# Performance work log

Measured on AMD Instinct MI355X. Metric: run time of the kernel, lower is better.

The kernel has to match this reference:

```python
import jax, jax.numpy as jnp
import numpy as np

B, C, N, H = 4, 512, 2048, 8
D = C // H  # per-head depth = 64
EPS = 1e-5


def conv1x1(x, W, b):
    # x: [B, Cin, N], W: [Cout, Cin], b: [Cout]
    return jnp.einsum('oc,bcn->bon', W, x) + b[None, :, None]


def instance_norm(x):
    # normalize over length dim per (batch, channel), no affine
    mu = jnp.mean(x, axis=-1, keepdims=True)
    var = jnp.var(x, axis=-1, keepdims=True)
    return (x - mu) * jax.lax.rsqrt(var + EPS)


def _pipeline(src, tgt, Wq, bq, Wk, bk, Wv, bv, Wm, bm):
    # query from src, key/value from tgt; reshape C -> (D outer, H inner)
    q = conv1x1(src, Wq, bq).reshape(B, D, H, N)
    k = conv1x1(tgt, Wk, bk).reshape(B, D, H, N)
    v = conv1x1(tgt, Wv, bv).reshape(B, D, H, N)
    scores = jnp.einsum('bdhn,bdhm->bhnm', q, k) / jnp.sqrt(jnp.float32(D))
    probs = jax.nn.softmax(scores, axis=-1)
    out = jnp.einsum('bhnm,bdhm->bdhn', probs, v).reshape(B, C, N)
    return conv1x1(out, Wm, bm)


def _mlp(x, W1, b1, W2, b2):
    h = conv1x1(x, W1, b1)
    h = jax.nn.relu(instance_norm(h))
    return conv1x1(h, W2, b2)


def setup_inputs() -> dict:
    key = jax.random.key(0)
    ks = jax.random.split(key, 8)
    s = 0.02
    return {
        'source_features': jax.random.normal(ks[0], (B, C, N), jnp.float32),
        'target_features': jax.random.normal(ks[1], (B, C, N), jnp.float32),
        'Wq': jax.random.normal(ks[2], (C, C), jnp.float32) * s,
        'bq': jnp.zeros((C,), jnp.float32),
        'Wk': jax.random.normal(ks[3], (C, C), jnp.float32) * s,
        'bk': jnp.zeros((C,), jnp.float32),
        'Wv': jax.random.normal(ks[4], (C, C), jnp.float32) * s,
        'bv': jnp.zeros((C,), jnp.float32),
        'Wm': jax.random.normal(ks[5], (C, C), jnp.float32) * s,
        'bm': jnp.zeros((C,), jnp.float32),
        'W1': jax.random.normal(ks[6], (2 * C, 2 * C), jnp.float32) * s,
        'b1': jnp.zeros((2 * C,), jnp.float32),
        'W2': jax.random.normal(ks[7], (C, 2 * C), jnp.float32) * s,
        'b2': jnp.zeros((C,), jnp.float32),
    }


def reference(source_features, target_features, Wq, bq, Wk, bk, Wv, bv, Wm, bm, W1, b1, W2, b2):
    src, tgt = source_features, target_features
    # source update uses ORIGINAL target features
    src_att = _pipeline(src, tgt, Wq, bq, Wk, bk, Wv, bv, Wm, bm)
    src = src + _mlp(jnp.concatenate([src, src_att], axis=1), W1, b1, W2, b2)
    # target update uses the UPDATED source features (in-place semantics of original)
    tgt_att = _pipeline(tgt, src, Wq, bq, Wk, bk, Wv, bv, Wm, bm)
    tgt = tgt + _mlp(jnp.concatenate([tgt, tgt_att], axis=1), W1, b1, W2, b2)
    return src, tgt
```

## Files before the change

kernel.cpp:

```cpp
#include <hip/hip_runtime.h>

#define NN 2048
#define CC 512
#define BB 4
#define HH 8
#define DD 64
#define SCALE 0.18033688011112043f

typedef unsigned short u16;
typedef __attribute__((ext_vector_type(8))) short bf16x8;
typedef __attribute__((ext_vector_type(4))) float f32x4;

extern "C" __device__ float __ocml_native_exp2_f32(float);

__device__ inline u16 f2b(float x) {
    unsigned u = __builtin_bit_cast(unsigned, x);
    u += 0x7fffu + ((u >> 16) & 1u);
    return (u16)(u >> 16);
}
__device__ inline float b2f(u16 h) {
    unsigned u = ((unsigned)h) << 16;
    return __builtin_bit_cast(float, u);
}

#define GLD16(g, l) __builtin_amdgcn_global_load_lds( \
    (const __attribute__((address_space(1))) unsigned int*)(g), \
    (__attribute__((address_space(3))) unsigned int*)(l), 16, 0, 0)

template<int JT>
__device__ __forceinline__ void gemm_core_t(
    const u16* __restrict__ Xa, const u16* __restrict__ Xb, int Ca, int K,
    const u16* __restrict__ Wt, size_t rowBase,
    u16* As, u16* Bs, f32x4 (&acc)[4][JT])
{
    constexpr int OT = JT * 32;
    const int tid = threadIdx.x;
    const int lane = tid & 63, w = tid >> 6;
    const int quad = lane >> 4, l16 = lane & 15;
    const int wrow = w & 1, wcol = w >> 1;
    const int arow = lane >> 3, aseg = lane & 7;
    const int asw = aseg ^ arow;
    const int lk = l16 & 7;

    for (int k0 = 0; k0 < K; k0 += 64) {
        const u16* Xs; int Crow, cc;
        if (k0 < Ca) { Xs = Xa; Crow = Ca; cc = k0; }
        else         { Xs = Xb; Crow = K - Ca; cc = k0 - Ca; }
#pragma unroll
        for (int i = 0; i < 4; ++i) {
            int rl = w * 32 + i * 8 + arow;
            int la = __builtin_amdgcn_readfirstlane((w * 32 + i * 8) * 64);
            GLD16(Xs + (rowBase + rl) * (size_t)Crow + cc + asw * 8, (char*)As + (size_t)la * 2);
        }
#pragma unroll
        for (int i = 0; i < OT / 32; ++i) {
            int rl = w * (OT / 4) + i * 8 + arow;
            int la = __builtin_amdgcn_readfirstlane((w * (OT / 4) + i * 8) * 64);
            GLD16(Wt + (size_t)rl * K + k0 + asw * 8, (char*)Bs + (size_t)la * 2);
        }
        __syncthreads();
#pragma unroll
        for (int kk = 0; kk < 2; ++kk) {
            const int g = ((kk * 4 + quad) ^ lk) * 8;
            bf16x8 av[4], bv[JT];
#pragma unroll
            for (int i = 0; i < 4; ++i)
                av[i] = *(const bf16x8*)&As[(wrow * 64 + i * 16 + l16) * 64 + g];
#pragma unroll
            for (int jj = 0; jj < JT; ++jj)
                bv[jj] = *(const bf16x8*)&Bs[(wcol * JT * 16 + jj * 16 + l16) * 64 + g];
#pragma unroll
            for (int i = 0; i < 4; ++i)
#pragma unroll
                for (int jj = 0; jj < JT; ++jj)
                    acc[i][jj] = __builtin_amdgcn_mfma_f32_16x16x32_bf16(av[i], bv[jj], acc[i][jj], 0, 0, 0);
        }
        __syncthreads();
    }
}

template<int JT>
__device__ __forceinline__ void gemm_epilogue_t(
    f32x4 (&acc)[4][JT], const float* __restrict__ bias, int mode,
    int b, int n0, int o0, int Cout,
    const float* __restrict__ res, float* __restrict__ outF, u16* __restrict__ outB)
{
    const int tid = threadIdx.x;
    const int lane = tid & 63, w = tid >> 6;
    const int quad = lane >> 4, l16 = lane & 15;
    const int wrow = w & 1, wcol = w >> 1;
    const size_t bN = (size_t)b * NN;
    const int nb0 = n0 + wrow * 64, ob0 = o0 + wcol * JT * 16;

    if (mode == 0) {
#pragma unroll
        for (int j = 0; j < JT; ++j) {
            int o = ob0 + j * 16 + l16;
            float bs = bias[o];
#pragma unroll
            for (int i = 0; i < 4; ++i)
#pragma unroll
                for (int r = 0; r < 4; ++r) {
                    int n = nb0 + i * 16 + quad * 4 + r;
                    outB[(bN + n) * Cout + o] = f2b(acc[i][j][r] + bs);
                }
        }
    } else if (mode == 1) {
#pragma unroll
        for (int j = 0; j < JT; ++j) {
            int o = ob0 + j * 16 + l16;
            float bs = bias[o];
            int h = o >> 6, d = o & 63;
#pragma unroll
            for (int i = 0; i < 4; ++i) {
                int n = nb0 + i * 16 + quad * 4;
                ushort4 pk;
                pk.x = f2b(acc[i][j][0] + bs); pk.y = f2b(acc[i][j][1] + bs);
                pk.z = f2b(acc[i][j][2] + bs); pk.w = f2b(acc[i][j][3] + bs);
                *(ushort4*)&outB[(((size_t)b * HH + h) * DD + d) * NN + n] = pk;
            }
        }
    } else {
#pragma unroll
        for (int j = 0; j < JT; ++j) {
            int o = ob0 + j * 16 + l16;
            float bs = bias[o];
#pragma unroll
            for (int i = 0; i < 4; ++i) {
                int n = nb0 + i * 16 + quad * 4;
                size_t ad = ((size_t)b * Cout + o) * NN + n;
                float4 rv = *(const float4*)&res[ad];
                float4 yv;
                yv.x = acc[i][j][0] + bs + rv.x;
                yv.y = acc[i][j][1] + bs + rv.y;
                yv.z = acc[i][j][2] + bs + rv.z;
                yv.w = acc[i][j][3] + bs + rv.w;
                *(float4*)&outF[ad] = yv;
                if (mode == 2) {
                    outB[(bN + n + 0) * Cout + o] = f2b(yv.x);
                    outB[(bN + n + 1) * Cout + o] = f2b(yv.y);
                    outB[(bN + n + 2) * Cout + o] = f2b(yv.z);
                    outB[(bN + n + 3) * Cout + o] = f2b(yv.w);
                }
            }
        }
    }
}

template<int JT>
__global__ __launch_bounds__(256, (JT == 2 ? 4 : 3)) void gemm_bf16_t(
    const u16* __restrict__ Wb, const float* __restrict__ bias,
    const u16* __restrict__ Xa, const u16* __restrict__ Xb,
    int Ca, int K, int Cout,
    const float* __restrict__ res, float* __restrict__ outF,
    u16* __restrict__ outB, int mode)
{
    __shared__ u16 As[128 * 64];
    __shared__ u16 Bs[JT * 32 * 64];
    const int b = blockIdx.z, n0 = blockIdx.x * 128, o0 = blockIdx.y * (JT * 32);
    f32x4 acc[4][JT] = {};
    gemm_core_t<JT>(Xa, Xb, Ca, K, Wb + (size_t)o0 * K, (size_t)b * NN + n0, As, Bs, acc);
    gemm_epilogue_t<JT>(acc, bias, mode, b, n0, o0, Cout, res, outF, outB);
}

__global__ __launch_bounds__(256, 3) void gemm_qkv(
    const u16* __restrict__ WQ, const float* __restrict__ bQ,
    const u16* __restrict__ XQ, u16* __restrict__ outQ,
    const u16* __restrict__ WK, const float* __restrict__ bK, u16* __restrict__ outK,
    const u16* __restrict__ WV, const float* __restrict__ bV, u16* __restrict__ outV,
    const u16* __restrict__ XKV)
{
    __shared__ u16 As[128 * 64];
    __shared__ u16 Bs[128 * 64];
    const int yb = blockIdx.y;
    const u16* W; const float* bias; const u16* X; u16* outB; int mode, o0;
    if (yb < 4)      { o0 = yb * 128;       W = WQ; bias = bQ; X = XQ;  outB = outQ; mode = 0; }
    else if (yb < 8) { o0 = (yb - 4) * 128; W = WK; bias = bK; X = XKV; outB = outK; mode = 0; }
    else             { o0 = (yb - 8) * 128; W = WV; bias = bV; X = XKV; outB = outV; mode = 1; }
    const int b = blockIdx.z, n0 = blockIdx.x * 128;
    f32x4 acc[4][4] = {};
    gemm_core_t<4>(X, nullptr, 512, 512, W + (size_t)o0 * 512, (size_t)b * NN + n0, As, Bs, acc);
    gemm_epilogue_t<4>(acc, bias, mode, b, n0, o0, 512, nullptr, nullptr, outB);
}

__global__ __launch_bounds__(512, 4) void attn(
    const u16* __restrict__ Qg, const u16* __restrict__ Kg,
    const u16* __restrict__ Vg, u16* __restrict__ Og)
{
    __shared__ __align__(16) u16 pool[6 * 4096];
    u16* const Ksb[2] = { pool, pool + 4096 };
    u16* const Vtb[2] = { pool + 2 * 4096, pool + 3 * 4096 };
    u16* const Ps = pool + 4 * 4096;
    const int tid = threadIdx.x;
    const int lane = tid & 63, w = tid >> 6;
    const int qg = w & 3, hv = w >> 2;
    const int quad = lane >> 4, l16 = lane & 15;
    const int id = blockIdx.x;
    const int xcd = id & 7, jj = id >> 3;
    const int bh = xcd * 4 + (jj >> 4), nb = jj & 15;
    const int b = bh >> 3, h = bh & 7;
    const int n0 = nb * 128, wn0 = qg * 32;
    const int sr0 = w * 8;
    const size_t qkBase = ((size_t)b * NN) * CC + h * DD;
    const size_t vBase  = (((size_t)b * HH + h) * DD) * NN;
    const int r8 = lane >> 3, seg = lane & 7;
    const int segp = seg ^ r8;
    const int lk = l16 & 7;

    const u16* kp = Kg + qkBase + (size_t)(sr0 + r8) * CC + segp * 8;
    const u16* vp = Vg + vBase + (size_t)(sr0 + r8) * NN + segp * 8;

    bf16x8 qf[2][2];
#pragma unroll
    for (int qs = 0; qs < 2; ++qs) {
        int n = n0 + wn0 + qs * 16 + l16;
#pragma unroll
        for (int ks = 0; ks < 2; ++ks)
            qf[qs][ks] = *(const bf16x8*)&Qg[qkBase + (size_t)n * CC + ks * 32 + quad * 8];
    }

    const short oneb = 0x3F80;
    const bf16x8 ones = {oneb, oneb, oneb, oneb, oneb, oneb, oneb, oneb};
    f32x4 oa[2][4] = {};
    f32x4 lacc[2] = {};

    GLD16(kp, Ksb[0] + sr0 * 64);
    GLD16(vp, Vtb[0] + sr0 * 64);
    kp += 64 * CC; vp += 64;

#define ATTN_PREF(BUF) do { \
        GLD16(kp, Ksb[BUF] + sr0 * 64); \
        GLD16(vp, Vtb[BUF] + sr0 * 64); \
        kp += 64 * CC; vp += 64; \
    } while (0)

#define ATTN_BODY(CUR) do { \
        const u16* ksb = Ksb[CUR]; \
        const u16* vtb = Vtb[CUR]; \
        f32x4 st[2][2] = {}; \
        _Pragma("unroll") \
        for (int ks = 0; ks < 2; ++ks) { \
            bf16x8 ak[2]; \
            _Pragma("unroll") \
            for (int rtl = 0; rtl < 2; ++rtl) \
                ak[rtl] = *(const bf16x8*)&ksb[(hv * 32 + rtl * 16 + l16) * 64 + ((ks * 4 + quad) ^ lk) * 8]; \
            __builtin_amdgcn_s_setprio(1); \
            _Pragma("unroll") \
            for (int rtl = 0; rtl < 2; ++rtl) \
                _Pragma("unroll") \
                for (int qs = 0; qs < 2; ++qs) \
                    st[qs][rtl] = __builtin_amdgcn_mfma_f32_16x16x32_bf16(ak[rtl], qf[qs][ks], st[qs][rtl], 0, 0, 0); \
            __builtin_amdgcn_s_setprio(0); \
        } \
        _Pragma("unroll") \
        for (int qs = 0; qs < 2; ++qs) { \
            int nrow = wn0 + qs * 16 + l16; \
            _Pragma("unroll") \
            for (int rtl = 0; rtl < 2; ++rtl) { \
                unsigned u0 = __builtin_bit_cast(unsigned, __ocml_native_exp2_f32(st[qs][rtl][0])); \
                unsigned u1 = __builtin_bit_cast(unsigned, __ocml_native_exp2_f32(st[qs][rtl][1])); \
                unsigned u2 = __builtin_bit_cast(unsigned, __ocml_native_exp2_f32(st[qs][rtl][2])); \
                unsigned u3 = __builtin_bit_cast(unsigned, __ocml_native_exp2_f32(st[qs][rtl][3])); \
                uint2 t; \
                t.x = __builtin_amdgcn_perm(u1, u0, 0x07060302u); \
                t.y = __builtin_amdgcn_perm(u3, u2, 0x07060302u); \
                int g = (((hv * 2 + rtl) * 2 + (quad >> 1))) ^ lk; \
                *(uint2*)&Ps[nrow * 64 + g * 8 + (quad & 1) * 4] = t; \
            } \
        } \
        { \
            bf16x8 pa[2]; \
            _Pragma("unroll") \
            for (int qs = 0; qs < 2; ++qs) \
                pa[qs] = *(const bf16x8*)&Ps[(wn0 + qs * 16 + l16) * 64 + ((hv * 4 + quad) ^ lk) * 8]; \
            bf16x8 vb[4]; \
            _Pragma("unroll") \
            for (int ct = 0; ct < 4; ++ct) \
                vb[ct] = *(const bf16x8*)&vtb[(ct * 16 + l16) * 64 + ((hv * 4 + quad) ^ lk) * 8]; \
            __builtin_amdgcn_s_setprio(1); \
            _Pragma("unroll") \
            for (int ct = 0; ct < 4; ++ct) \
                _Pragma("unroll") \
                for (int qs = 0; qs < 2; ++qs) \
                    oa[qs][ct] = __builtin_amdgcn_mfma_f32_16x16x32_bf16(pa[qs], vb[ct], oa[qs][ct], 0, 0, 0); \
            _Pragma("unroll") \
            for (int qs = 0; qs < 2; ++qs) \
                lacc[qs] = __builtin_amdgcn_mfma_f32_16x16x32_bf16(pa[qs], ones, lacc[qs], 0, 0, 0); \
            __builtin_amdgcn_s_setprio(0); \
        } \
    } while (0)

    for (int it = 0; it < NN / 64; it += 2) {
        __syncthreads();
        ATTN_PREF(1);
        ATTN_BODY(0);
        __syncthreads();
        if (it < NN / 64 - 2)
            ATTN_PREF(0);
        ATTN_BODY(1);
    }
#undef ATTN_PREF
#undef ATTN_BODY

    __syncthreads();
    float* M = (float*)pool;
    const int mbase = (qg * 64 + lane) * 40;
    if (hv == 1) {
#pragma unroll
        for (int qs = 0; qs < 2; ++qs)
#pragma unroll
            for (int ct = 0; ct < 4; ++ct)
                *(f32x4*)&M[mbase + (qs * 4 + ct) * 4] = oa[qs][ct];
        *(f32x4*)&M[mbase + 32] = lacc[0];
        *(f32x4*)&M[mbase + 36] = lacc[1];
    }
    __syncthreads();
    if (hv == 0) {
#pragma unroll
        for (int qs = 0; qs < 2; ++qs)
#pragma unroll
            for (int ct = 0; ct < 4; ++ct)
                oa[qs][ct] += *(const f32x4*)&M[mbase + (qs * 4 + ct) * 4];
        lacc[0] += *(const f32x4*)&M[mbase + 32];
        lacc[1] += *(const f32x4*)&M[mbase + 36];
#pragma unroll
        for (int qs = 0; qs < 2; ++qs)
#pragma unroll
            for (int r = 0; r < 4; ++r) {
                float li = 1.f / lacc[qs][r];
                int n = n0 + wn0 + qs * 16 + quad * 4 + r;
#pragma unroll
                for (int ct = 0; ct < 4; ++ct)
                    Og[qkBase + (size_t)n * CC + ct * 16 + l16] = f2b(oa[qs][ct][r] * li);
            }
    }
}

__global__ __launch_bounds__(256) void transpose_cvt(
    const float* __restrict__ X, u16* __restrict__ Y)
{
    __shared__ float T[64][65];
    const int tid = threadIdx.x;
    const int n0 = blockIdx.x * 64, c0 = blockIdx.y * 64, b = blockIdx.z;
    const int rr = tid >> 4, cc4 = tid & 15;
#pragma unroll
    for (int p = 0; p < 4; ++p) {
        int cl = p * 16 + rr;
        float4 v = *(const float4*)&X[((size_t)b * CC + c0 + cl) * NN + n0 + cc4 * 4];
        T[cl][cc4 * 4 + 0] = v.x; T[cl][cc4 * 4 + 1] = v.y;
        T[cl][cc4 * 4 + 2] = v.z; T[cl][cc4 * 4 + 3] = v.w;
    }
    __syncthreads();
#pragma unroll
    for (int p = 0; p < 4; ++p) {
        int nl = p * 16 + rr;
        ushort4 pk;
        pk.x = f2b(T[cc4 * 4 + 0][nl]);
        pk.y = f2b(T[cc4 * 4 + 1][nl]);
        pk.z = f2b(T[cc4 * 4 + 2][nl]);
        pk.w = f2b(T[cc4 * 4 + 3][nl]);
        *(ushort4*)&Y[((size_t)b * NN + n0 + nl) * CC + c0 + cc4 * 4] = pk;
    }
}

__global__ __launch_bounds__(256) void prep_weights(
    const float* __restrict__ Wq, const float* __restrict__ Wk,
    const float* __restrict__ Wv, const float* __restrict__ Wm,
    const float* __restrict__ W1, const float* __restrict__ W2,
    u16* oQ, u16* oK, u16* oV, u16* oM, u16* o1, u16* o2)
{
    const float* W; u16* o; int rows, cols, perm; float sc = 1.f;
    switch (blockIdx.z) {
        case 0: W = Wq; o = oQ; rows = 512;  cols = 512;  perm = 1; sc = SCALE; break;
        case 1: W = Wk; o = oK; rows = 512;  cols = 512;  perm = 1; break;
        case 2: W = Wv; o = oV; rows = 512;  cols = 512;  perm = 1; break;
        case 3: W = Wm; o = oM; rows = 512;  cols = 512;  perm = 2; break;
        case 4: W = W1; o = o1; rows = 1024; cols = 1024; perm = 0; break;
        default: W = W2; o = o2; rows = 512; cols = 1024; perm = 0; break;
    }
    int c = blockIdx.x * 256 + threadIdx.x;
    int r = blockIdx.y;
    if (r >= rows || c >= cols) return;
    int sr = r, scol = c;
    if (perm == 1) sr = (r & 63) * 8 + (r >> 6);
    else if (perm == 2) scol = (c & 63) * 8 + (c >> 6);
    o[(size_t)r * cols + c] = f2b(W[(size_t)sr * cols + scol] * sc);
}

__global__ void prep_bias(const float* __restrict__ bq, const float* __restrict__ bk,
                          const float* __restrict__ bv,
                          float* oq, float* ok, float* ov)
{
    int i = blockIdx.x * 256 + threadIdx.x;
    int y = blockIdx.y;
    const float* s = (y == 0) ? bq : (y == 1) ? bk : bv;
    float* o = (y == 0) ? oq : (y == 1) ? ok : ov;
    float v = s[(i & 63) * 8 + (i >> 6)];
    if (y == 0) v *= SCALE;
    o[i] = v;
}

__global__ __launch_bounds__(256) void inorm_p1(
    const u16* __restrict__ X, float* __restrict__ Ssum, float* __restrict__ Ssq)
{
    __shared__ float rs[4][64], rq[4][64];
    const int tid = threadIdx.x;
    const int cl = tid & 63, g = tid >> 6;
    const int c = blockIdx.x * 64 + cl;
    const int b = blockIdx.y, nz = blockIdx.z;
    float s = 0.f, q = 0.f;
    size_t base = ((size_t)b * NN + nz * 256 + g * 64) * 1024 + c;
#pragma unroll 4
    for (int i = 0; i < 64; ++i) {
        float x = b2f(X[base + (size_t)i * 1024]);
        s += x; q += x * x;
    }
    rs[g][cl] = s; rq[g][cl] = q;
    __syncthreads();
    if (g == 0) {
        s = rs[0][cl] + rs[1][cl] + rs[2][cl] + rs[3][cl];
        q = rq[0][cl] + rq[1][cl] + rq[2][cl] + rq[3][cl];
        atomicAdd(&Ssum[b * 1024 + c], s);
        atomicAdd(&Ssq[b * 1024 + c], q);
    }
}

__global__ __launch_bounds__(256) void inorm_p2(
    u16* __restrict__ X, const float* __restrict__ Ssum, const float* __restrict__ Ssq)
{
    const int tid = threadIdx.x;
    const int cl = tid & 63, g = tid >> 6;
    const int c = blockIdx.x * 64 + cl;
    const int b = blockIdx.y, nz = blockIdx.z;
    float mean = Ssum[b * 1024 + c] * (1.f / NN);
    float var  = Ssq[b * 1024 + c] * (1.f / NN) - mean * mean;
    float rstd = rsqrtf(fmaxf(var, 0.f) + 1e-5f);
    size_t base = ((size_t)b * NN + nz * 256 + g * 64) * 1024 + c;
#pragma unroll 4
    for (int i = 0; i < 64; ++i) {
        float x = b2f(X[base + (size_t)i * 1024]);
        x = (x - mean) * rstd;
        X[base + (size_t)i * 1024] = f2b(fmaxf(x, 0.f));
    }
}

extern "C" void kernel_launch(void* const* d_in, const int* in_sizes, int n_in,
                              void* d_out, int out_size, void* d_ws, size_t ws_size,
                              hipStream_t stream)
{
    (void)in_sizes; (void)n_in; (void)out_size; (void)ws_size;
    const float* src = (const float*)d_in[0];
    const float* tgt = (const float*)d_in[1];
    const float* Wq = (const float*)d_in[2];  const float* bq = (const float*)d_in[3];
    const float* Wk = (const float*)d_in[4];  const float* bk = (const float*)d_in[5];
    const float* Wv = (const float*)d_in[6];  const float* bv = (const float*)d_in[7];
    const float* Wm = (const float*)d_in[8];  const float* bm = (const float*)d_in[9];
    const float* W1 = (const float*)d_in[10]; const float* b1 = (const float*)d_in[11];
    const float* W2 = (const float*)d_in[12]; const float* b2 = (const float*)d_in[13];

    char* w = (char*)d_ws;
    u16* WQp = (u16*)(w);
    u16* WKp = (u16*)(w + (512u << 10));
    u16* WVp = (u16*)(w + (1u << 20));
    u16* WMp = (u16*)(w + (3u << 19));
    u16* W1b = (u16*)(w + (2u << 20));
    u16* W2b = (u16*)(w + (4u << 20));
    float* BQp = (float*)(w + (5u << 20));
    float* BKp = BQp + 512;
    float* BVp = BQp + 1024;
    float* STS = BQp + 1536;
    float* STQ = STS + 4096;
    u16* X0 = (u16*)(w + ( 6u << 20));
    u16* X1 = (u16*)(w + (14u << 20));
    u16* B0 = (u16*)(w + (22u << 20));
    u16* B1 = (u16*)(w + (30u << 20));
    u16* B2 = (u16*)(w + (38u << 20));
    u16* B3 = (u16*)(w + (46u << 20));

    float* out = (float*)d_out;
    const size_t R = (size_t)BB * CC * NN;
    dim3 blk(256), blkA(512);

    prep_weights<<<dim3(4, 1024, 6), blk, 0, stream>>>(Wq, Wk, Wv, Wm, W1, W2,
                                                       WQp, WKp, WVp, WMp, W1b, W2b);
    prep_bias<<<dim3(2, 3), blk, 0, stream>>>(bq, bk, bv, BQp, BKp, BVp);
    transpose_cvt<<<dim3(32, 8, 4), blk, 0, stream>>>(src, X0);
    transpose_cvt<<<dim3(32, 8, 4), blk, 0, stream>>>(tgt, X1);

    dim3 gQKV(16, 12, 4), gM(16, 8, 4), gW1(16, 8, 4), gW2(16, 8, 4);

    gemm_qkv<<<gQKV, blk, 0, stream>>>(WQp, BQp, X0, B0, WKp, BKp, B1, WVp, BVp, B2, X1);
    attn<<<dim3(512), blkA, 0, stream>>>(B0, B1, B2, B3);
    gemm_bf16_t<2><<<gM, blk, 0, stream>>>(WMp, bm, B3, nullptr, 512, 512, 512, nullptr, nullptr, B0, 0);
    gemm_bf16_t<4><<<gW1, blk, 0, stream>>>(W1b, b1, X0, B0, 512, 1024, 1024, nullptr, nullptr, B1, 0);
    hipMemsetAsync(STS, 0, 8192 * sizeof(float), stream);
    inorm_p1<<<dim3(16, 4, 8), blk, 0, stream>>>(B1, STS, STQ);
    inorm_p2<<<dim3(16, 4, 8), blk, 0, stream>>>(B1, STS, STQ);
    gemm_bf16_t<2><<<gW2, blk, 0, stream>>>(W2b, b2, B1, nullptr, 1024, 1024, 512, src, out, B3, 2);

    gemm_qkv<<<gQKV, blk, 0, stream>>>(WQp, BQp, X1, X0, WKp, BKp, B0, WVp, BVp, B1, B3);
    attn<<<dim3(512), blkA, 0, stream>>>(X0, B0, B1, B2);
    gemm_bf16_t<2><<<gM, blk, 0, stream>>>(WMp, bm, B2, nullptr, 512, 512, 512, nullptr, nullptr, X0, 0);
    gemm_bf16_t<4><<<gW1, blk, 0, stream>>>(W1b, b1, X1, X0, 512, 1024, 1024, nullptr, nullptr, B0, 0);
    hipMemsetAsync(STS, 0, 8192 * sizeof(float), stream);
    inorm_p1<<<dim3(16, 4, 8), blk, 0, stream>>>(B0, STS, STQ);
    inorm_p2<<<dim3(16, 4, 8), blk, 0, stream>>>(B0, STS, STQ);
    gemm_bf16_t<2><<<gW2, blk, 0, stream>>>(W2b, b2, B0, nullptr, 1024, 1024, 512, tgt, out + R, nullptr, 3);
}
```

Measured before the change: 399.3 us.

## Load K/V fragments directly from global into registers in attention loop

```diff
diff --git a/kernel.cpp b/kernel.cpp
--- a/kernel.cpp
+++ b/kernel.cpp
@@ -187,10 +187,8 @@
     const u16* __restrict__ Qg, const u16* __restrict__ Kg,
     const u16* __restrict__ Vg, u16* __restrict__ Og)
 {
-    __shared__ __align__(16) u16 pool[6 * 4096];
-    u16* const Ksb[2] = { pool, pool + 4096 };
-    u16* const Vtb[2] = { pool + 2 * 4096, pool + 3 * 4096 };
-    u16* const Ps = pool + 4 * 4096;
+    __shared__ __align__(16) float Mg[4 * 64 * 41];
+    u16* const Ps = (u16*)Mg;
     const int tid = threadIdx.x;
     const int lane = tid & 63, w = tid >> 6;
     const int qg = w & 3, hv = w >> 2;
@@ -200,15 +198,12 @@
     const int bh = xcd * 4 + (jj >> 4), nb = jj & 15;
     const int b = bh >> 3, h = bh & 7;
     const int n0 = nb * 128, wn0 = qg * 32;
-    const int sr0 = w * 8;
     const size_t qkBase = ((size_t)b * NN) * CC + h * DD;
     const size_t vBase  = (((size_t)b * HH + h) * DD) * NN;
-    const int r8 = lane >> 3, seg = lane & 7;
-    const int segp = seg ^ r8;
     const int lk = l16 & 7;
 
-    const u16* kp = Kg + qkBase + (size_t)(sr0 + r8) * CC + segp * 8;
-    const u16* vp = Vg + vBase + (size_t)(sr0 + r8) * NN + segp * 8;
+    const u16* kb = Kg + qkBase + (size_t)(hv * 32 + l16) * CC + quad * 8;
+    const u16* vbp = Vg + vBase + (size_t)l16 * NN + hv * 32 + quad * 8;
 
     bf16x8 qf[2][2];
 #pragma unroll
@@ -224,95 +219,75 @@
     f32x4 oa[2][4] = {};
     f32x4 lacc[2] = {};
 
-    GLD16(kp, Ksb[0] + sr0 * 64);
-    GLD16(vp, Vtb[0] + sr0 * 64);
-    kp += 64 * CC; vp += 64;
-
-#define ATTN_PREF(BUF) do { \
-        GLD16(kp, Ksb[BUF] + sr0 * 64); \
-        GLD16(vp, Vtb[BUF] + sr0 * 64); \
-        kp += 64 * CC; vp += 64; \
-    } while (0)
-
-#define ATTN_BODY(CUR) do { \
-        const u16* ksb = Ksb[CUR]; \
-        const u16* vtb = Vtb[CUR]; \
-        f32x4 st[2][2] = {}; \
-        _Pragma("unroll") \
-        for (int ks = 0; ks < 2; ++ks) { \
-            bf16x8 ak[2]; \
-            _Pragma("unroll") \
-            for (int rtl = 0; rtl < 2; ++rtl) \
-                ak[rtl] = *(const bf16x8*)&ksb[(hv * 32 + rtl * 16 + l16) * 64 + ((ks * 4 + quad) ^ lk) * 8]; \
-            __builtin_amdgcn_s_setprio(1); \
-            _Pragma("unroll") \
-            for (int rtl = 0; rtl < 2; ++rtl) \
-                _Pragma("unroll") \
-                for (int qs = 0; qs < 2; ++qs) \
-                    st[qs][rtl] = __builtin_amdgcn_mfma_f32_16x16x32_bf16(ak[rtl], qf[qs][ks], st[qs][rtl], 0, 0, 0); \
-            __builtin_amdgcn_s_setprio(0); \
-        } \
-        _Pragma("unroll") \
-        for (int qs = 0; qs < 2; ++qs) { \
-            int nrow = wn0 + qs * 16 + l16; \
-            _Pragma("unroll") \
-            for (int rtl = 0; rtl < 2; ++rtl) { \
-                unsigned u0 = __builtin_bit_cast(unsigned, __ocml_native_exp2_f32(st[qs][rtl][0])); \
-                unsigned u1 = __builtin_bit_cast(unsigned, __ocml_native_exp2_f32(st[qs][rtl][1])); \
-                unsigned u2 = __builtin_bit_cast(unsigned, __ocml_native_exp2_f32(st[qs][rtl][2])); \
-                unsigned u3 = __builtin_bit_cast(unsigned, __ocml_native_exp2_f32(st[qs][rtl][3])); \
-                uint2 t; \
-                t.x = __builtin_amdgcn_perm(u1, u0, 0x07060302u); \
-                t.y = __builtin_amdgcn_perm(u3, u2, 0x07060302u); \
-                int g = (((hv * 2 + rtl) * 2 + (quad >> 1))) ^ lk; \
-                *(uint2*)&Ps[nrow * 64 + g * 8 + (quad & 1) * 4] = t; \
-            } \
-        } \
-        { \
-            bf16x8 pa[2]; \
-            _Pragma("unroll") \
-            for (int qs = 0; qs < 2; ++qs) \
-                pa[qs] = *(const bf16x8*)&Ps[(wn0 + qs * 16 + l16) * 64 + ((hv * 4 + quad) ^ lk) * 8]; \
-            bf16x8 vb[4]; \
-            _Pragma("unroll") \
-            for (int ct = 0; ct < 4; ++ct) \
-                vb[ct] = *(const bf16x8*)&vtb[(ct * 16 + l16) * 64 + ((hv * 4 + quad) ^ lk) * 8]; \
-            __builtin_amdgcn_s_setprio(1); \
-            _Pragma("unroll") \
-            for (int ct = 0; ct < 4; ++ct) \
-                _Pragma("unroll") \
-                for (int qs = 0; qs < 2; ++qs) \
-                    oa[qs][ct] = __builtin_amdgcn_mfma_f32_16x16x32_bf16(pa[qs], vb[ct], oa[qs][ct], 0, 0, 0); \
-            _Pragma("unroll") \
-            for (int qs = 0; qs < 2; ++qs) \
-                lacc[qs] = __builtin_amdgcn_mfma_f32_16x16x32_bf16(pa[qs], ones, lacc[qs], 0, 0, 0); \
-            __builtin_amdgcn_s_setprio(0); \
-        } \
-    } while (0)
-
-    for (int it = 0; it < NN / 64; it += 2) {
-        __syncthreads();
-        ATTN_PREF(1);
-        ATTN_BODY(0);
-        __syncthreads();
-        if (it < NN / 64 - 2)
-            ATTN_PREF(0);
-        ATTN_BODY(1);
-    }
-#undef ATTN_PREF
-#undef ATTN_BODY
+    for (int it = 0; it < NN / 64; ++it) {
+        bf16x8 ak[2][2];
+#pragma unroll
+        for (int ks = 0; ks < 2; ++ks)
+#pragma unroll
+            for (int rtl = 0; rtl < 2; ++rtl)
+                ak[ks][rtl] = *(const bf16x8*)&kb[(size_t)(rtl * 16) * CC + ks * 32];
+        bf16x8 vb[4];
+#pragma unroll
+        for (int ct = 0; ct < 4; ++ct)
+            vb[ct] = *(const bf16x8*)&vbp[(size_t)(ct * 16) * NN];
+        kb += (size_t)64 * CC; vbp += 64;
+
+        f32x4 st[2][2] = {};
+        __builtin_amdgcn_s_setprio(1);
+#pragma unroll
+        for (int ks = 0; ks < 2; ++ks)
+#pragma unroll
+            for (int rtl = 0; rtl < 2; ++rtl)
+#pragma unroll
+                for (int qs = 0; qs < 2; ++qs)
+                    st[qs][rtl] = __builtin_amdgcn_mfma_f32_16x16x32_bf16(ak[ks][rtl], qf[qs][ks], st[qs][rtl], 0, 0, 0);
+        __builtin_amdgcn_s_setprio(0);
+
+#pragma unroll
+        for (int qs = 0; qs < 2; ++qs) {
+            int nrow = wn0 + qs * 16 + l16;
+#pragma unroll
+            for (int rtl = 0; rtl < 2; ++rtl) {
+                unsigned u0 = __builtin_bit_cast(unsigned, __ocml_native_exp2_f32(st[qs][rtl][0]));
+                unsigned u1 = __builtin_bit_cast(unsigned, __ocml_native_exp2_f32(st[qs][rtl][1]));
+                unsigned u2 = __builtin_bit_cast(unsigned, __ocml_native_exp2_f32(st[qs][rtl][2]));
+                unsigned u3 = __builtin_bit_cast(unsigned, __ocml_native_exp2_f32(st[qs][rtl][3]));
+                uint2 t;
+                t.x = __builtin_amdgcn_perm(u1, u0, 0x07060302u);
+                t.y = __builtin_amdgcn_perm(u3, u2, 0x07060302u);
+                int g = (((hv * 2 + rtl) * 2 + (quad >> 1))) ^ lk;
+                *(uint2*)&Ps[nrow * 64 + g * 8 + (quad & 1) * 4] = t;
+            }
+        }
+
+        {
+            bf16x8 pa[2];
+#pragma unroll
+            for (int qs = 0; qs < 2; ++qs)
+                pa[qs] = *(const bf16x8*)&Ps[(wn0 + qs * 16 + l16) * 64 + ((hv * 4 + quad) ^ lk) * 8];
+            __builtin_amdgcn_s_setprio(1);
+#pragma unroll
+            for (int ct = 0; ct < 4; ++ct)
+#pragma unroll
+                for (int qs = 0; qs < 2; ++qs)
+                    oa[qs][ct] = __builtin_amdgcn_mfma_f32_16x16x32_bf16(pa[qs], vb[ct], oa[qs][ct], 0, 0, 0);
+#pragma unroll
+            for (int qs = 0; qs < 2; ++qs)
+                lacc[qs] = __builtin_amdgcn_mfma_f32_16x16x32_bf16(pa[qs], ones, lacc[qs], 0, 0, 0);
+            __builtin_amdgcn_s_setprio(0);
+        }
+    }
 
     __syncthreads();
-    float* M = (float*)pool;
-    const int mbase = (qg * 64 + lane) * 40;
+    const int mbase = (qg * 64 + lane) * 41;
     if (hv == 1) {
 #pragma unroll
         for (int qs = 0; qs < 2; ++qs)
 #pragma unroll
             for (int ct = 0; ct < 4; ++ct)
-                *(f32x4*)&M[mbase + (qs * 4 + ct) * 4] = oa[qs][ct];
-        *(f32x4*)&M[mbase + 32] = lacc[0];
-        *(f32x4*)&M[mbase + 36] = lacc[1];
+                *(f32x4*)&Mg[mbase + (qs * 4 + ct) * 4] = oa[qs][ct];
+        *(f32x4*)&Mg[mbase + 32] = lacc[0];
+        *(f32x4*)&Mg[mbase + 36] = lacc[1];
     }
     __syncthreads();
     if (hv == 0) {
@@ -320,9 +295,9 @@
         for (int qs = 0; qs < 2; ++qs)
 #pragma unroll
             for (int ct = 0; ct < 4; ++ct)
-                oa[qs][ct] += *(const f32x4*)&M[mbase + (qs * 4 + ct) * 4];
-        lacc[0] += *(const f32x4*)&M[mbase + 32];
-        lacc[1] += *(const f32x4*)&M[mbase + 36];
+                oa[qs][ct] += *(const f32x4*)&Mg[mbase + (qs * 4 + ct) * 4];
+        lacc[0] += *(const f32x4*)&Mg[mbase + 32];
+        lacc[1] += *(const f32x4*)&Mg[mbase + 36];
 #pragma unroll
         for (int qs = 0; qs < 2; ++qs)
 #pragma unroll
```

New measurement: 563.6 us. 41.2% more time.

## Double-buffer LDS tiles in generic GEMM and pad attention merge stride

Applied to the files above, without the earlier changes.

```diff
diff --git a/kernel.cpp b/kernel.cpp
--- a/kernel.cpp
+++ b/kernel.cpp
@@ -27,13 +27,14 @@
     (const __attribute__((address_space(1))) unsigned int*)(g), \
     (__attribute__((address_space(3))) unsigned int*)(l), 16, 0, 0)
 
-template<int JT>
+template<int JT, bool DBUF>
 __device__ __forceinline__ void gemm_core_t(
     const u16* __restrict__ Xa, const u16* __restrict__ Xb, int Ca, int K,
     const u16* __restrict__ Wt, size_t rowBase,
     u16* As, u16* Bs, f32x4 (&acc)[4][JT])
 {
     constexpr int OT = JT * 32;
+    constexpr int ASZ = 128 * 64, BSZ = OT * 64;
     const int tid = threadIdx.x;
     const int lane = tid & 63, w = tid >> 6;
     const int quad = lane >> 4, l16 = lane & 15;
@@ -42,7 +43,7 @@
     const int asw = aseg ^ arow;
     const int lk = l16 & 7;
 
-    for (int k0 = 0; k0 < K; k0 += 64) {
+    auto stage = [&](int k0, u16* Ad, u16* Bd) {
         const u16* Xs; int Crow, cc;
         if (k0 < Ca) { Xs = Xa; Crow = Ca; cc = k0; }
         else         { Xs = Xb; Crow = K - Ca; cc = k0 - Ca; }
@@ -50,32 +51,52 @@
         for (int i = 0; i < 4; ++i) {
             int rl = w * 32 + i * 8 + arow;
             int la = __builtin_amdgcn_readfirstlane((w * 32 + i * 8) * 64);
-            GLD16(Xs + (rowBase + rl) * (size_t)Crow + cc + asw * 8, (char*)As + (size_t)la * 2);
+            GLD16(Xs + (rowBase + rl) * (size_t)Crow + cc + asw * 8, (char*)Ad + (size_t)la * 2);
         }
 #pragma unroll
         for (int i = 0; i < OT / 32; ++i) {
             int rl = w * (OT / 4) + i * 8 + arow;
             int la = __builtin_amdgcn_readfirstlane((w * (OT / 4) + i * 8) * 64);
-            GLD16(Wt + (size_t)rl * K + k0 + asw * 8, (char*)Bs + (size_t)la * 2);
-        }
-        __syncthreads();
+            GLD16(Wt + (size_t)rl * K + k0 + asw * 8, (char*)Bd + (size_t)la * 2);
+        }
+    };
+    auto compute = [&](const u16* Ac, const u16* Bc) {
 #pragma unroll
         for (int kk = 0; kk < 2; ++kk) {
             const int g = ((kk * 4 + quad) ^ lk) * 8;
             bf16x8 av[4], bv[JT];
 #pragma unroll
             for (int i = 0; i < 4; ++i)
-                av[i] = *(const bf16x8*)&As[(wrow * 64 + i * 16 + l16) * 64 + g];
+                av[i] = *(const bf16x8*)&Ac[(wrow * 64 + i * 16 + l16) * 64 + g];
 #pragma unroll
             for (int jj = 0; jj < JT; ++jj)
-                bv[jj] = *(const bf16x8*)&Bs[(wcol * JT * 16 + jj * 16 + l16) * 64 + g];
+                bv[jj] = *(const bf16x8*)&Bc[(wcol * JT * 16 + jj * 16 + l16) * 64 + g];
 #pragma unroll
             for (int i = 0; i < 4; ++i)
 #pragma unroll
                 for (int jj = 0; jj < JT; ++jj)
                     acc[i][jj] = __builtin_amdgcn_mfma_f32_16x16x32_bf16(av[i], bv[jj], acc[i][jj], 0, 0, 0);
         }
-        __syncthreads();
+    };
+
+    if constexpr (DBUF) {
+        stage(0, As, Bs);
+        const int nt = K / 64;
+        for (int t = 0; t < nt; ++t) {
+            const u16* Ac = As + (t & 1) * ASZ;
+            const u16* Bc = Bs + (t & 1) * BSZ;
+            __syncthreads();
+            if (t + 1 < nt)
+                stage((t + 1) * 64, As + ((t + 1) & 1) * ASZ, Bs + ((t + 1) & 1) * BSZ);
+            compute(Ac, Bc);
+        }
+    } else {
+        for (int k0 = 0; k0 < K; k0 += 64) {
+            stage(k0, As, Bs);
+            __syncthreads();
+            compute(As, Bs);
+            __syncthreads();
+        }
     }
 }
 
@@ -148,18 +169,18 @@
 }
 
 template<int JT>
-__global__ __launch_bounds__(256, (JT == 2 ? 4 : 3)) void gemm_bf16_t(
+__global__ __launch_bounds__(256, (JT == 2 ? 3 : 2)) void gemm_bf16_t(
     const u16* __restrict__ Wb, const float* __restrict__ bias,
     const u16* __restrict__ Xa, const u16* __restrict__ Xb,
     int Ca, int K, int Cout,
     const float* __restrict__ res, float* __restrict__ outF,
     u16* __restrict__ outB, int mode)
 {
-    __shared__ u16 As[128 * 64];
-    __shared__ u16 Bs[JT * 32 * 64];
+    __shared__ u16 As[2 * 128 * 64];
+    __shared__ u16 Bs[2 * JT * 32 * 64];
     const int b = blockIdx.z, n0 = blockIdx.x * 128, o0 = blockIdx.y * (JT * 32);
     f32x4 acc[4][JT] = {};
-    gemm_core_t<JT>(Xa, Xb, Ca, K, Wb + (size_t)o0 * K, (size_t)b * NN + n0, As, Bs, acc);
+    gemm_core_t<JT, true>(Xa, Xb, Ca, K, Wb + (size_t)o0 * K, (size_t)b * NN + n0, As, Bs, acc);
     gemm_epilogue_t<JT>(acc, bias, mode, b, n0, o0, Cout, res, outF, outB);
 }
 
@@ -179,7 +200,7 @@
     else             { o0 = (yb - 8) * 128; W = WV; bias = bV; X = XKV; outB = outV; mode = 1; }
     const int b = blockIdx.z, n0 = blockIdx.x * 128;
     f32x4 acc[4][4] = {};
-    gemm_core_t<4>(X, nullptr, 512, 512, W + (size_t)o0 * 512, (size_t)b * NN + n0, As, Bs, acc);
+    gemm_core_t<4, false>(X, nullptr, 512, 512, W + (size_t)o0 * 512, (size_t)b * NN + n0, As, Bs, acc);
     gemm_epilogue_t<4>(acc, bias, mode, b, n0, o0, 512, nullptr, nullptr, outB);
 }
 
@@ -304,7 +325,7 @@
 
     __syncthreads();
     float* M = (float*)pool;
-    const int mbase = (qg * 64 + lane) * 40;
+    const int mbase = (qg * 64 + lane) * 41;
     if (hv == 1) {
 #pragma unroll
         for (int qs = 0; qs < 2; ++qs)
```

Result: no change. 401.8 us (+0.6%).
